# Kernel tuning notes

Hardware: AMD Instinct MI355X
Metric: run time of the kernel (lower is better)

The kernel has to match this reference:

```python
import jax, jax.numpy as jnp
import numpy as np


def setup_inputs() -> dict:
    key = jax.random.key(0)
    k1, k2 = jax.random.split(key)
    B, N, M = 8, 8192, 8192
    preds = jax.random.normal(k1, (B, N, 3), dtype=jnp.float32)
    gts = jax.random.normal(k2, (B, M, 3), dtype=jnp.float32)
    return {"preds": preds, "gts": gts}


def _pairwise_sqdist(x, y):
    # x: [B, Nx, 3], y: [B, Ny, 3] -> P[b, i, j] = ||x_i - y_j||^2
    xx = jnp.sum(x * x, axis=-1)                      # [B, Nx]
    yy = jnp.sum(y * y, axis=-1)                      # [B, Ny]
    zz = jnp.einsum("bnd,bmd->bnm", x, y)            # [B, Nx, Ny]
    return xx[:, :, None] + yy[:, None, :] - 2.0 * zz


def reference(preds, gts):
    # matches forward with use_mask=False, reduce=False
    P = _pairwise_sqdist(gts, preds)                  # [B, M_gt, N_pred]
    loss_1 = jnp.mean(jnp.min(P, axis=1), axis=-1)    # min over gt points
    loss_2 = jnp.mean(jnp.min(P, axis=2), axis=-1)    # min over pred points
    return loss_1 + loss_2                            # [B]
```

## Files before the change

kernel.cpp:

```cpp
#include <hip/hip_runtime.h>

#define TPB 512
#define QPT 8
#define NSEG 32

__device__ __forceinline__ unsigned encf(float f) {
    unsigned u = __float_as_uint(f);
    return (u & 0x80000000u) ? ~u : (u | 0x80000000u);
}
__device__ __forceinline__ float decf(unsigned u) {
    return __uint_as_float((u & 0x80000000u) ? (u ^ 0x80000000u) : ~u);
}

__global__ void __launch_bounds__(256) prep(const float* __restrict__ preds,
                                            const float* __restrict__ gts,
                                            float4* __restrict__ P4,
                                            float4* __restrict__ G4,
                                            unsigned* __restrict__ umins,
                                            int totalP, int totalG, int totalU) {
    int i = blockIdx.x * blockDim.x + threadIdx.x;
    if (i < totalP) {
        float x = preds[3 * i], y = preds[3 * i + 1], z = preds[3 * i + 2];
        P4[i] = make_float4(x, y, z, fmaf(x, x, fmaf(y, y, z * z)));
    } else if (i < totalP + totalG) {
        int k = i - totalP;
        float x = gts[3 * k], y = gts[3 * k + 1], z = gts[3 * k + 2];
        G4[k] = make_float4(x, y, z, fmaf(x, x, fmaf(y, y, z * z)));
    }
    if (i < totalU) umins[i] = 0xFFFFFFFFu;
}

__global__ void __launch_bounds__(TPB, 8) chamfer_dir(const float4* __restrict__ P4,
                                                      const float4* __restrict__ G4,
                                                      unsigned* __restrict__ umins,
                                                      int N, int M, int B, int nQpad) {
    const int db  = blockIdx.z;
    const int dir = db / B;
    const int b   = db - dir * B;
    const int seg = blockIdx.y;

    const float4* __restrict__ Q = (dir == 0) ? (P4 + (size_t)b * N) : (G4 + (size_t)b * M);
    const float4* __restrict__ R = (dir == 0) ? (G4 + (size_t)b * M) : (P4 + (size_t)b * N);
    const int nQ = (dir == 0) ? N : M;
    const int nR = (dir == 0) ? M : N;

    const int segLen = (nR + NSEG - 1) / NSEG;
    const int s0 = seg * segLen;
    const int s1 = (s0 + segLen < nR) ? (s0 + segLen) : nR;
    if (s0 >= s1) return;

    const int qbase = blockIdx.x * (TPB * QPT) + (int)threadIdx.x;

    float q2x[QPT], q2y[QPT], q2z[QPT], qw[QPT], m[QPT];
    #pragma unroll
    for (int j = 0; j < QPT; ++j) {
        const int q  = qbase + j * TPB;
        const int qc = (q < nQ) ? q : 0;
        float4 t = Q[qc];
        q2x[j] = -2.f * t.x;
        q2y[j] = -2.f * t.y;
        q2z[j] = -2.f * t.z;
        qw[j]  = t.w;
        m[j]   = 3.4e38f;
    }

#define PAIR(rr, jj)  fmaf(q2x[jj], (rr).x, fmaf(q2y[jj], (rr).y, fmaf(q2z[jj], (rr).z, (rr).w)))

    int i = s0;
    if (s1 - s0 >= 8) {
        float4 r0 = R[i + 0], r1 = R[i + 1], r2 = R[i + 2], r3 = R[i + 3];
        for (; i + 8 <= s1; i += 4) {
            float4 n0 = R[i + 4], n1 = R[i + 5], n2 = R[i + 6], n3 = R[i + 7];
            #pragma unroll
            for (int j = 0; j < QPT; ++j) {
                float d0 = PAIR(r0, j);
                float d1 = PAIR(r1, j);
                float d2 = PAIR(r2, j);
                float d3 = PAIR(r3, j);
                m[j] = fminf(fminf(m[j], d0), d1);
                m[j] = fminf(fminf(m[j], d2), d3);
            }
            r0 = n0; r1 = n1; r2 = n2; r3 = n3;
        }
        #pragma unroll
        for (int j = 0; j < QPT; ++j) {
            float d0 = PAIR(r0, j);
            float d1 = PAIR(r1, j);
            float d2 = PAIR(r2, j);
            float d3 = PAIR(r3, j);
            m[j] = fminf(fminf(m[j], d0), d1);
            m[j] = fminf(fminf(m[j], d2), d3);
        }
        i += 4;
    }
    for (; i < s1; ++i) {
        float4 r = R[i];
        #pragma unroll
        for (int j = 0; j < QPT; ++j) m[j] = fminf(m[j], PAIR(r, j));
    }
#undef PAIR

    unsigned* dst = umins + (size_t)db * nQpad;
    #pragma unroll
    for (int j = 0; j < QPT; ++j) {
        const int q = qbase + j * TPB;
        if (q < nQ) atomicMin(&dst[q], encf(m[j] + qw[j]));
    }
}

__global__ void __launch_bounds__(256) finish(const unsigned* __restrict__ umins,
                                              float* __restrict__ out,
                                              int N, int M, int B, int nQpad) {
    const int b = blockIdx.x;
    const unsigned* m0 = umins + (size_t)b * nQpad;
    const unsigned* m1 = umins + (size_t)(B + b) * nQpad;

    float s0 = 0.f, s1 = 0.f;
    for (int q = (int)threadIdx.x; q < N; q += 256) s0 += decf(m0[q]);
    for (int q = (int)threadIdx.x; q < M; q += 256) s1 += decf(m1[q]);

    for (int off = 32; off > 0; off >>= 1) {
        s0 += __shfl_down(s0, off);
        s1 += __shfl_down(s1, off);
    }
    __shared__ float r0s[4], r1s[4];
    const int wid  = (int)threadIdx.x >> 6;
    const int lane = (int)threadIdx.x & 63;
    if (lane == 0) { r0s[wid] = s0; r1s[wid] = s1; }
    __syncthreads();
    if (threadIdx.x == 0) {
        float S0 = 0.f, S1 = 0.f;
        #pragma unroll
        for (int w = 0; w < 4; ++w) { S0 += r0s[w]; S1 += r1s[w]; }
        out[b] = S0 / (float)N + S1 / (float)M;
    }
}

extern "C" void kernel_launch(void* const* d_in, const int* in_sizes, int n_in,
                              void* d_out, int out_size, void* d_ws, size_t ws_size,
                              hipStream_t stream) {
    const float* preds = (const float*)d_in[0];
    const float* gts   = (const float*)d_in[1];
    float* out = (float*)d_out;

    const int B = out_size;
    const int N = in_sizes[0] / (B * 3);
    const int M = in_sizes[1] / (B * 3);
    const int nQpad = (N > M ? N : M);

    float4*   P4    = (float4*)d_ws;
    float4*   G4    = P4 + (size_t)B * N;
    unsigned* umins = (unsigned*)(G4 + (size_t)B * M);

    const int totalP = B * N;
    const int totalG = B * M;
    const int totalU = 2 * B * nQpad;
    const int prepTot = (totalP + totalG > totalU) ? (totalP + totalG) : totalU;
    prep<<<(prepTot + 255) / 256, 256, 0, stream>>>(preds, gts, P4, G4, umins,
                                                    totalP, totalG, totalU);

    const int qChunks = (nQpad + TPB * QPT - 1) / (TPB * QPT);
    dim3 grid(qChunks, NSEG, 2 * B);
    chamfer_dir<<<grid, TPB, 0, stream>>>(P4, G4, umins, N, M, B, nQpad);

    finish<<<B, 256, 0, stream>>>(umins, out, N, M, B, nQpad);
}
```

Measured before the change: 126.0 us.

## Use packed FP32 FMA with duplicated reference coordinates from scalar registers

Reference points are stored as duplicated float pairs (32 bytes each), so each coordinate can be fed as a 64-bit scalar operand to v_pk_fma_f32 through inline asm. Two query points are processed per packed FMA, which halves the FMA instruction count in the inner loop. The min updates stay scalar. This doubles reference-point memory and workspace size, lowers the launch_bounds occupancy hint from 8 to 4, and relies on the reference loads being uniform so they land in SGPRs.

After: 107.6 us. 14.6% less time.

```diff
diff --git a/kernel.cpp b/kernel.cpp
--- a/kernel.cpp
+++ b/kernel.cpp
@@ -2,7 +2,12 @@
 
 #define TPB 512
 #define QPT 8
+#define NCH (QPT / 2)
 #define NSEG 32
+
+typedef float v2f __attribute__((ext_vector_type(2)));
+
+struct RefDup { double x2, y2, z2, w2; };
 
 __device__ __forceinline__ unsigned encf(float f) {
     unsigned u = __float_as_uint(f);
@@ -11,27 +16,40 @@
 __device__ __forceinline__ float decf(unsigned u) {
     return __uint_as_float((u & 0x80000000u) ? (u ^ 0x80000000u) : ~u);
 }
+__device__ __forceinline__ double dup2(float v) {
+    union { float f[2]; double d; } u; u.f[0] = v; u.f[1] = v; return u.d;
+}
+
+__device__ __forceinline__ v2f pk_fma_vs(v2f a, double b, v2f c) {
+    v2f d; asm("v_pk_fma_f32 %0, %1, %2, %3" : "=v"(d) : "v"(a), "s"(b), "v"(c)); return d;
+}
 
 __global__ void __launch_bounds__(256) prep(const float* __restrict__ preds,
                                             const float* __restrict__ gts,
-                                            float4* __restrict__ P4,
-                                            float4* __restrict__ G4,
+                                            RefDup* __restrict__ P8,
+                                            RefDup* __restrict__ G8,
                                             unsigned* __restrict__ umins,
                                             int totalP, int totalG, int totalU) {
     int i = blockIdx.x * blockDim.x + threadIdx.x;
     if (i < totalP) {
         float x = preds[3 * i], y = preds[3 * i + 1], z = preds[3 * i + 2];
-        P4[i] = make_float4(x, y, z, fmaf(x, x, fmaf(y, y, z * z)));
+        RefDup r;
+        r.x2 = dup2(x); r.y2 = dup2(y); r.z2 = dup2(z);
+        r.w2 = dup2(fmaf(x, x, fmaf(y, y, z * z)));
+        P8[i] = r;
     } else if (i < totalP + totalG) {
         int k = i - totalP;
         float x = gts[3 * k], y = gts[3 * k + 1], z = gts[3 * k + 2];
-        G4[k] = make_float4(x, y, z, fmaf(x, x, fmaf(y, y, z * z)));
+        RefDup r;
+        r.x2 = dup2(x); r.y2 = dup2(y); r.z2 = dup2(z);
+        r.w2 = dup2(fmaf(x, x, fmaf(y, y, z * z)));
+        G8[k] = r;
     }
     if (i < totalU) umins[i] = 0xFFFFFFFFu;
 }
 
-__global__ void __launch_bounds__(TPB, 8) chamfer_dir(const float4* __restrict__ P4,
-                                                      const float4* __restrict__ G4,
+__global__ void __launch_bounds__(TPB, 4) chamfer_dir(const RefDup* __restrict__ P8,
+                                                      const RefDup* __restrict__ G8,
                                                       unsigned* __restrict__ umins,
                                                       int N, int M, int B, int nQpad) {
     const int db  = blockIdx.z;
@@ -39,8 +57,8 @@
     const int b   = db - dir * B;
     const int seg = blockIdx.y;
 
-    const float4* __restrict__ Q = (dir == 0) ? (P4 + (size_t)b * N) : (G4 + (size_t)b * M);
-    const float4* __restrict__ R = (dir == 0) ? (G4 + (size_t)b * M) : (P4 + (size_t)b * N);
+    const RefDup* __restrict__ Qd = (dir == 0) ? (P8 + (size_t)b * N) : (G8 + (size_t)b * M);
+    const RefDup* __restrict__ R  = (dir == 0) ? (G8 + (size_t)b * M) : (P8 + (size_t)b * N);
     const int nQ = (dir == 0) ? N : M;
     const int nR = (dir == 0) ? M : N;
 
@@ -51,60 +69,82 @@
 
     const int qbase = blockIdx.x * (TPB * QPT) + (int)threadIdx.x;
 
-    float q2x[QPT], q2y[QPT], q2z[QPT], qw[QPT], m[QPT];
+    v2f qx2[NCH], qy2[NCH], qz2[NCH], pw2[NCH], m2[NCH];
     #pragma unroll
-    for (int j = 0; j < QPT; ++j) {
-        const int q  = qbase + j * TPB;
-        const int qc = (q < nQ) ? q : 0;
-        float4 t = Q[qc];
-        q2x[j] = -2.f * t.x;
-        q2y[j] = -2.f * t.y;
-        q2z[j] = -2.f * t.z;
-        qw[j]  = t.w;
-        m[j]   = 3.4e38f;
-    }
-
-#define PAIR(rr, jj)  fmaf(q2x[jj], (rr).x, fmaf(q2y[jj], (rr).y, fmaf(q2z[jj], (rr).z, (rr).w)))
+    for (int c = 0; c < NCH; ++c) {
+        const int qa = qbase + (2 * c) * TPB;
+        const int qb = qbase + (2 * c + 1) * TPB;
+        const int qac = (qa < nQ) ? qa : 0;
+        const int qbc = (qb < nQ) ? qb : 0;
+        const float* fa = (const float*)&Qd[qac];
+        const float* fb = (const float*)&Qd[qbc];
+        qx2[c].x = -2.f * fa[0]; qx2[c].y = -2.f * fb[0];
+        qy2[c].x = -2.f * fa[2]; qy2[c].y = -2.f * fb[2];
+        qz2[c].x = -2.f * fa[4]; qz2[c].y = -2.f * fb[4];
+        pw2[c].x = fa[6];        pw2[c].y = fb[6];
+        m2[c].x = 3.4e38f;       m2[c].y = 3.4e38f;
+    }
+
+    auto dupw = [](double w) -> v2f {
+        union { double d; float f[2]; } u; u.d = w;
+        v2f r; r.x = u.f[0]; r.y = u.f[1]; return r;
+    };
+
+    auto step4 = [&](const RefDup& r0, const RefDup& r1,
+                     const RefDup& r2, const RefDup& r3) {
+        v2f w0 = dupw(r0.w2), w1 = dupw(r1.w2), w2v = dupw(r2.w2), w3 = dupw(r3.w2);
+        #pragma unroll
+        for (int c = 0; c < NCH; ++c) {
+            v2f d0 = pk_fma_vs(qz2[c], r0.z2, w0);
+            d0 = pk_fma_vs(qy2[c], r0.y2, d0);
+            d0 = pk_fma_vs(qx2[c], r0.x2, d0);
+            v2f d1 = pk_fma_vs(qz2[c], r1.z2, w1);
+            d1 = pk_fma_vs(qy2[c], r1.y2, d1);
+            d1 = pk_fma_vs(qx2[c], r1.x2, d1);
+            v2f d2 = pk_fma_vs(qz2[c], r2.z2, w2v);
+            d2 = pk_fma_vs(qy2[c], r2.y2, d2);
+            d2 = pk_fma_vs(qx2[c], r2.x2, d2);
+            v2f d3 = pk_fma_vs(qz2[c], r3.z2, w3);
+            d3 = pk_fma_vs(qy2[c], r3.y2, d3);
+            d3 = pk_fma_vs(qx2[c], r3.x2, d3);
+            m2[c].x = fminf(fminf(m2[c].x, d0.x), d1.x);
+            m2[c].y = fminf(fminf(m2[c].y, d0.y), d1.y);
+            m2[c].x = fminf(fminf(m2[c].x, d2.x), d3.x);
+            m2[c].y = fminf(fminf(m2[c].y, d2.y), d3.y);
+        }
+    };
 
     int i = s0;
     if (s1 - s0 >= 8) {
-        float4 r0 = R[i + 0], r1 = R[i + 1], r2 = R[i + 2], r3 = R[i + 3];
+        RefDup r0 = R[i], r1 = R[i + 1], r2 = R[i + 2], r3 = R[i + 3];
         for (; i + 8 <= s1; i += 4) {
-            float4 n0 = R[i + 4], n1 = R[i + 5], n2 = R[i + 6], n3 = R[i + 7];
-            #pragma unroll
-            for (int j = 0; j < QPT; ++j) {
-                float d0 = PAIR(r0, j);
-                float d1 = PAIR(r1, j);
-                float d2 = PAIR(r2, j);
-                float d3 = PAIR(r3, j);
-                m[j] = fminf(fminf(m[j], d0), d1);
-                m[j] = fminf(fminf(m[j], d2), d3);
-            }
+            RefDup n0 = R[i + 4], n1 = R[i + 5], n2 = R[i + 6], n3 = R[i + 7];
+            step4(r0, r1, r2, r3);
             r0 = n0; r1 = n1; r2 = n2; r3 = n3;
         }
+        step4(r0, r1, r2, r3);
+        i += 4;
+    }
+    for (; i < s1; ++i) {
+        RefDup r = R[i];
+        v2f wv = dupw(r.w2);
         #pragma unroll
-        for (int j = 0; j < QPT; ++j) {
-            float d0 = PAIR(r0, j);
-            float d1 = PAIR(r1, j);
-            float d2 = PAIR(r2, j);
-            float d3 = PAIR(r3, j);
-            m[j] = fminf(fminf(m[j], d0), d1);
-            m[j] = fminf(fminf(m[j], d2), d3);
+        for (int c = 0; c < NCH; ++c) {
+            v2f d = pk_fma_vs(qz2[c], r.z2, wv);
+            d = pk_fma_vs(qy2[c], r.y2, d);
+            d = pk_fma_vs(qx2[c], r.x2, d);
+            m2[c].x = fminf(m2[c].x, d.x);
+            m2[c].y = fminf(m2[c].y, d.y);
         }
-        i += 4;
-    }
-    for (; i < s1; ++i) {
-        float4 r = R[i];
-        #pragma unroll
-        for (int j = 0; j < QPT; ++j) m[j] = fminf(m[j], PAIR(r, j));
-    }
-#undef PAIR
-
-    unsigned* dst = umins + (size_t)db * nQpad;
+    }
+
+    unsigned* __restrict__ dst = umins + (size_t)db * nQpad;
     #pragma unroll
-    for (int j = 0; j < QPT; ++j) {
-        const int q = qbase + j * TPB;
-        if (q < nQ) atomicMin(&dst[q], encf(m[j] + qw[j]));
+    for (int c = 0; c < NCH; ++c) {
+        const int qa = qbase + (2 * c) * TPB;
+        const int qb = qbase + (2 * c + 1) * TPB;
+        if (qa < nQ) atomicMin(&dst[qa], encf(m2[c].x + pw2[c].x));
+        if (qb < nQ) atomicMin(&dst[qb], encf(m2[c].y + pw2[c].y));
     }
 }
 
@@ -148,20 +188,20 @@
     const int M = in_sizes[1] / (B * 3);
     const int nQpad = (N > M ? N : M);
 
-    float4*   P4    = (float4*)d_ws;
-    float4*   G4    = P4 + (size_t)B * N;
-    unsigned* umins = (unsigned*)(G4 + (size_t)B * M);
+    RefDup*   P8    = (RefDup*)d_ws;
+    RefDup*   G8    = P8 + (size_t)B * N;
+    unsigned* umins = (unsigned*)(G8 + (size_t)B * M);
 
     const int totalP = B * N;
     const int totalG = B * M;
     const int totalU = 2 * B * nQpad;
     const int prepTot = (totalP + totalG > totalU) ? (totalP + totalG) : totalU;
-    prep<<<(prepTot + 255) / 256, 256, 0, stream>>>(preds, gts, P4, G4, umins,
+    prep<<<(prepTot + 255) / 256, 256, 0, stream>>>(preds, gts, P8, G8, umins,
                                                     totalP, totalG, totalU);
 
     const int qChunks = (nQpad + TPB * QPT - 1) / (TPB * QPT);
     dim3 grid(qChunks, NSEG, 2 * B);
-    chamfer_dir<<<grid, TPB, 0, stream>>>(P4, G4, umins, N, M, B, nQpad);
+    chamfer_dir<<<grid, TPB, 0, stream>>>(P8, G8, umins, N, M, B, nQpad);
 
     finish<<<B, 256, 0, stream>>>(umins, out, N, M, B, nQpad);
 }
```
